# Kernel optimization log

Hardware: AMD Instinct MI355X
Metric: run time of the kernel (lower is better)

## Reference

```python
import jax, jax.numpy as jnp
import numpy as np

N_TYPES = 4
NEG_SLOPE = 0.01


def _conv(x, row, col, edge_type, edge_weight, W, b):
    # x: [N, d_in], W: [4, d_in, d_out], b: [d_out]
    N = x.shape[0]
    # in-degree based symmetric normalization (deg counted on col, as in source)
    deg = jax.ops.segment_sum(jnp.ones(col.shape[0], dtype=x.dtype), col, num_segments=N)
    deg_inv_sqrt = jnp.where(deg > 0, deg ** -0.5, jnp.zeros((), x.dtype))
    norm = deg_inv_sqrt[row] * deg_inv_sqrt[col] * edge_weight  # [E]
    # project all nodes by each of the 4 relation weights, then gather per edge
    # (equivalent to per-edge bmm x[col] @ W[edge_type], but avoids [E,d,d])
    xw = jnp.einsum('ni,tio->tno', x, W)          # [4, N, d_out]
    x_j = xw[edge_type, col] * norm[:, None]      # [E, d_out]
    out = jax.ops.segment_sum(x_j, row, num_segments=N) + b  # [N, d_out]
    # dropout omitted (eval mode / deterministic reference)
    return jax.nn.leaky_relu(out, negative_slope=NEG_SLOPE)


def setup_inputs() -> dict:
    key = jax.random.key(0)
    ks = jax.random.split(key, 10)
    N, d, E = 50000, 128, 625000
    x = jax.random.normal(ks[0], (N, d), dtype=jnp.float32)
    edge_index = jax.random.randint(ks[1], (2, E), 0, N, dtype=jnp.int64 if jax.config.jax_enable_x64 else jnp.int32)
    edge_type = jax.random.randint(ks[2], (E,), 0, N_TYPES)
    edge_attr = jax.random.uniform(ks[3], (E,), dtype=jnp.float32)
    # xavier_uniform for (4, d, d): gain=1, bound = sqrt(6/(d+d))
    bound = float(np.sqrt(6.0 / (d + d)))
    W1 = jax.random.uniform(ks[4], (N_TYPES, d, d), minval=-bound, maxval=bound, dtype=jnp.float32)
    W2 = jax.random.uniform(ks[5], (N_TYPES, d, d), minval=-bound, maxval=bound, dtype=jnp.float32)
    W3 = jax.random.uniform(ks[6], (N_TYPES, d, d), minval=-bound, maxval=bound, dtype=jnp.float32)
    b1 = jnp.zeros((d,), jnp.float32)
    b2 = jnp.zeros((d,), jnp.float32)
    b3 = jnp.zeros((d,), jnp.float32)
    return {"x": x, "edge_index": edge_index, "edge_type": edge_type, "edge_attr": edge_attr,
            "W1": W1, "b1": b1, "W2": W2, "b2": b2, "W3": W3, "b3": b3}


def reference(x, edge_index, edge_type, edge_attr, W1, b1, W2, b2, W3, b3):
    row, col = edge_index[0], edge_index[1]
    z1 = _conv(x, row, col, edge_type, edge_attr, W1, b1)
    z2 = _conv(z1, row, col, edge_type, edge_attr, W2, b2)
    z3 = _conv(z2, row, col, edge_type, edge_attr, W3, b3)
    return (x + z1 + z2 + z3) / 4
```

## Files before the change

### kernel.cpp

```cpp
#include <hip/hip_runtime.h>

#define DIM 128
#define SLOTS 64

typedef __attribute__((ext_vector_type(8))) short bf16x8;
typedef __attribute__((ext_vector_type(4))) float f32x4;
typedef __attribute__((ext_vector_type(2))) float f32x2;
typedef unsigned short u16;
typedef unsigned int u32;
typedef unsigned long long u64;

__device__ __forceinline__ float bf2f(u32 u) {
    return __builtin_bit_cast(float, u << 16);
}
__device__ __forceinline__ u16 f2bf(float f) {
    u32 u = __builtin_bit_cast(u32, f);
    u = (u + 0x7FFFu + ((u >> 16) & 1u)) >> 16;
    return (u16)u;
}
__device__ __forceinline__ u32 pack2bf(float a, float b) {
    return (u32)f2bf(a) | ((u32)f2bf(b) << 16);
}


__global__ __launch_bounds__(1024) void k_hist(const int* __restrict__ col, int E,
                                               int* __restrict__ part, int N) {
    __shared__ int hist[12544];
    int b = blockIdx.x;
    int range = b >> 3;
    int chunk = b & 7;
    int quarter = (N + 3) >> 2;
    int base = range * quarter;
    int hn = N - base; if (hn > quarter) hn = quarter;
    for (int i = threadIdx.x; i < hn; i += 1024) hist[i] = 0;
    __syncthreads();
    int e0 = (int)((long long)chunk * E / 8);
    int e1 = (int)((long long)(chunk + 1) * E / 8);
    for (int e = e0 + threadIdx.x; e < e1; e += 1024) {
        int c = col[e] - base;
        if ((u32)c < (u32)hn) atomicAdd(&hist[c], 1);
    }
    __syncthreads();
    int* dst = part + (size_t)b * quarter;
    for (int i = threadIdx.x; i < hn; i += 1024) dst[i] = hist[i];
}

__global__ void k_dis2(const int* __restrict__ part, float* __restrict__ dis, int N) {
    int i = blockIdx.x * 256 + threadIdx.x;
    if (i >= N) return;
    int quarter = (N + 3) >> 2;
    int range = i / quarter;
    int il = i - range * quarter;
    const int* p = part + ((size_t)range * 8) * quarter + il;
    int s = 0;
    #pragma unroll
    for (int b = 0; b < 8; b++) s += p[(size_t)b * quarter];
    dis[i] = s > 0 ? rsqrtf((float)s) : 0.f;
}


__global__ __launch_bounds__(256) void k_setup(const int* __restrict__ row, const int* __restrict__ col,
                                               const int* __restrict__ et, const float* __restrict__ ew,
                                               int E, int* __restrict__ fill,
                                               u64* __restrict__ ep,
                                               const float* __restrict__ x, u16* __restrict__ xb, int nx4,
                                               const float* __restrict__ W1, const float* __restrict__ W2,
                                               const float* __restrict__ W3,
                                               u16* __restrict__ Wt1, u16* __restrict__ Wt2,
                                               u16* __restrict__ Wt3, int nEb, int nXb) {
    int b = blockIdx.x, tid = threadIdx.x;
    if (b < nEb) {
        int e0 = (b * 256 + tid) * 4;
        #pragma unroll
        for (int i = 0; i < 4; i++) {
            int e = e0 + i;
            if (e < E) {
                int r = row[e], c = col[e];
                int pos = atomicAdd(&fill[r], 1);
                if (pos < SLOTS)
                    ep[(size_t)r * SLOTS + pos] =
                        ((u64)__builtin_bit_cast(u32, ew[e]) << 32) | (u32)((c << 8) | et[e]);
            }
        }
    } else if (b < nEb + nXb) {
        int i = (b - nEb) * 256 + tid;
        if (i < nx4) {
            float4 v = ((const float4*)x)[i];
            ushort4 o;
            o.x = f2bf(v.x); o.y = f2bf(v.y); o.z = f2bf(v.z); o.w = f2bf(v.w);
            ((ushort4*)xb)[i] = o;
        }
    } else {
        int b2 = b - nEb - nXb;
        const float* W = b2 < 256 ? W1 : (b2 < 512 ? W2 : W3);
        u16* Wt = b2 < 256 ? Wt1 : (b2 < 512 ? Wt2 : Wt3);
        int o = (b2 & 255) * 256 + tid;
        int chunk = o >> 10;
        int c = (o >> 3) & 127;
        int k = chunk * 8 + (o & 7);
        Wt[o] = f2bf(W[(k >> 7) * 16384 + (k & 127) * 128 + c]);
    }
}


__global__ __launch_bounds__(256) void k_norm(const int* __restrict__ fill,
                                              const float* __restrict__ dis,
                                              u64* __restrict__ ep, int N) {
    int wid = threadIdx.x >> 6, lane = threadIdx.x & 63;
    int n = blockIdx.x * 4 + wid;
    if (n >= N) return;
    int cnt = fill[n]; if (cnt > SLOTS) cnt = SLOTS;
    int padded = (cnt + 7) & ~7;
    float dn = dis[n];
    u64* eb = ep + (size_t)n * SLOTS;
    if (lane < cnt) {
        u64 q = eb[lane];
        u32 lo = (u32)q;
        float wgt = __builtin_bit_cast(float, (u32)(q >> 32)) * dn * dis[lo >> 8];
        eb[lane] = ((u64)__builtin_bit_cast(u32, wgt) << 32) | lo;
    } else if (lane < padded) {
        eb[lane] = 0;
    }
}


template <int MODE>
__global__ __launch_bounds__(1024, 2) void k_layer(const u16* __restrict__ src,
                                                   const int* __restrict__ fill,
                                                   const u64* __restrict__ ep,
                                                   const u16* __restrict__ Wt,
                                                   const float* __restrict__ bias,
                                                   const float* __restrict__ x0,
                                                   const u16* __restrict__ z1b,
                                                   const u16* __restrict__ z2b,
                                                   float* __restrict__ outf,
                                                   u16* __restrict__ outb, int N) {
    __shared__ u16 sA[16 * 512];
    int tid = threadIdx.x, wid = tid >> 6, lane = tid & 63;
    int n0 = blockIdx.x * 16;
    int n = n0 + wid;

    f32x2 a0 = {0.f, 0.f}, a1 = {0.f, 0.f}, a2 = {0.f, 0.f}, a3 = {0.f, 0.f};
    int cnt = 0;
    if (n < N) {
        cnt = fill[n];
        if (cnt > SLOTS) cnt = SLOTS;
    }
    u64 myq = ep[(size_t)n * SLOTS + lane];
    u32 mylo = (u32)myq;
    u32 mywu = (u32)(myq >> 32);
    const char* srcc = (const char*)src;

#define RL(x, i_) ((u32)__builtin_amdgcn_readlane((int)(x), (i_)))

#define EDGE(lo_, wu_, v_) { \
        float w_  = __builtin_bit_cast(float, (u32)(wu_)); \
        f32x2 vv_; \
        vv_[0] = __builtin_bit_cast(float, (v_) << 16); \
        vv_[1] = __builtin_bit_cast(float, (v_) & 0xFFFF0000u); \
        u32 t_ = (u32)(lo_) & 3u; \
        float w0_ = t_ == 0u ? w_ : 0.f; \
        float w1_ = t_ == 1u ? w_ : 0.f; \
        float w2_ = t_ == 2u ? w_ : 0.f; \
        float w3_ = t_ == 3u ? w_ : 0.f; \
        a0 = __builtin_elementwise_fma(vv_, (f32x2){w0_, w0_}, a0); \
        a1 = __builtin_elementwise_fma(vv_, (f32x2){w1_, w1_}, a1); \
        a2 = __builtin_elementwise_fma(vv_, (f32x2){w2_, w2_}, a2); \
        a3 = __builtin_elementwise_fma(vv_, (f32x2){w3_, w3_}, a3); }

    for (int j = 0; j < cnt; j += 8) {
        u32 lo[8], wu[8], v[8];
        #pragma unroll
        for (int i = 0; i < 8; i++) {
            lo[i] = RL(mylo, j + i);
            wu[i] = RL(mywu, j + i);
        }
        #pragma unroll
        for (int i = 0; i < 8; i++) {
            const u32* rowp = (const u32*)(srcc + (lo[i] & 0xFFFFFF00u));
            v[i] = rowp[lane];
        }
        #pragma unroll
        for (int i = 0; i < 8; i++)
            EDGE(lo[i], wu[i], v[i]);
    }
#undef EDGE
#undef RL

    {
        u32 X = (u32)((wid & 7) << 4);
        char* base = (char*)sA + wid * 1024;
        *(u32*)(base + ((lane * 4 + 0  ) ^ X)) = pack2bf(a0[0], a0[1]);
        *(u32*)(base + ((lane * 4 + 256) ^ X)) = pack2bf(a1[0], a1[1]);
        *(u32*)(base + ((lane * 4 + 512) ^ X)) = pack2bf(a2[0], a2[1]);
        *(u32*)(base + ((lane * 4 + 768) ^ X)) = pack2bf(a3[0], a3[1]);
    }
    __syncthreads();

    if (wid < 8) {
        int lr = lane & 15, lk = lane >> 4;
        u32 X = (u32)((lr & 7) << 4);
        const char* ab = (const char*)sA + lr * 1024;
        const u16* bb = Wt + lk * 1024 + (wid * 16 + lr) * 8;
        f32x4 acc = {};
        #pragma unroll
        for (int ks = 0; ks < 16; ks++) {
            bf16x8 af = *(const bf16x8*)(ab + ((ks * 64 + lk * 16) ^ X));
            bf16x8 bfv = *(const bf16x8*)(bb + ks * 4096);
            acc = __builtin_amdgcn_mfma_f32_16x16x32_bf16(af, bfv, acc, 0, 0, 0);
        }

        int colg = wid * 16 + lr;
        float bv = bias[colg];
        #pragma unroll
        for (int r = 0; r < 4; r++) {
            int nn = n0 + lk * 4 + r;
            if (nn < N) {
                size_t idx = (size_t)nn * DIM + colg;
                float v = acc[r] + bv;
                v = v > 0.f ? v : 0.01f * v;
                if (MODE == 1)
                    outf[idx] = 0.25f * (x0[idx] + bf2f(z1b[idx]) + bf2f(z2b[idx]) + v);
                else
                    outb[idx] = f2bf(v);
            }
        }
    }
}


extern "C" void kernel_launch(void* const* d_in, const int* in_sizes, int n_in,
                              void* d_out, int out_size, void* d_ws, size_t ws_size,
                              hipStream_t stream) {
    const float* x     = (const float*)d_in[0];
    const int*   eidx  = (const int*)d_in[1];
    const int*   etype = (const int*)d_in[2];
    const float* eattr = (const float*)d_in[3];
    const float* W1 = (const float*)d_in[4];
    const float* b1 = (const float*)d_in[5];
    const float* W2 = (const float*)d_in[6];
    const float* b2 = (const float*)d_in[7];
    const float* W3 = (const float*)d_in[8];
    const float* b3 = (const float*)d_in[9];

    const int E = in_sizes[2];
    const int N = in_sizes[0] / DIM;
    const int* row = eidx;
    const int* col = eidx + E;

    char* w = (char*)d_ws;
    size_t off = 0;
    auto alloc = [&](size_t bytes) { size_t o = off; off = (off + bytes + 255) & ~255ULL; return o; };
    int*   fill = (int*)(w + alloc((size_t)N * 4));
    float* dis  = (float*)(w + alloc((size_t)N * 4));
    int    quarter = (N + 3) >> 2;
    int*   part = (int*)(w + alloc((size_t)32 * quarter * 4));
    u64*   ep   = (u64*)(w + alloc((size_t)N * SLOTS * 8));
    u16*   xb   = (u16*)(w + alloc((size_t)N * DIM * 2));
    u16*   z1b  = (u16*)(w + alloc((size_t)N * DIM * 2));
    u16*   z2b  = (u16*)(w + alloc((size_t)N * DIM * 2));
    u16*   Wt1  = (u16*)(w + alloc(65536 * 2));
    u16*   Wt2  = (u16*)(w + alloc(65536 * 2));
    u16*   Wt3  = (u16*)(w + alloc(65536 * 2));

    hipMemsetAsync(fill, 0, (size_t)N * 4, stream);

    int nx4 = N * DIM / 4;
    int nEb = (E + 1023) / 1024;
    int nXb = (nx4 + 255) / 256;

    k_hist<<<32, 1024, 0, stream>>>(col, E, part, N);
    k_dis2<<<(N + 255) / 256, 256, 0, stream>>>(part, dis, N);
    k_setup<<<nEb + nXb + 768, 256, 0, stream>>>(row, col, etype, eattr, E, fill, ep,
                                                 x, xb, nx4, W1, W2, W3, Wt1, Wt2, Wt3, nEb, nXb);
    k_norm<<<(N + 3) / 4, 256, 0, stream>>>(fill, dis, ep, N);

    int grid = (N + 15) / 16;
    k_layer<0><<<grid, 1024, 0, stream>>>(xb,  fill, ep, Wt1, b1, nullptr, nullptr, nullptr, nullptr, z1b, N);
    k_layer<0><<<grid, 1024, 0, stream>>>(z1b, fill, ep, Wt2, b2, nullptr, nullptr, nullptr, nullptr, z2b, N);
    k_layer<1><<<grid, 1024, 0, stream>>>(z2b, fill, ep, Wt3, b3, x, z1b, z2b, (float*)d_out, nullptr, N);
}
```

Measured before the change: 234.5 us.

## Sort nodes by padded in-degree so each layer block gets balanced work

Adds a counting sort (bin, scan, place kernels) that orders nodes by their padded edge count in groups of 8. Each 16-node layer block then processes nodes with similar degree, which cuts wave imbalance inside a block before the shared-memory sync and MFMA. Output rows are scattered through the order table. This costs three extra small kernels and the loss of contiguous output rows, which weakens locality for the writes and the residual reads.

New measurement: 237.1 us. About the same (+1.1%).

```diff
diff --git a/kernel.cpp b/kernel.cpp
--- a/kernel.cpp
+++ b/kernel.cpp
@@ -123,10 +123,56 @@
     }
 }
 
+__global__ __launch_bounds__(256) void k_bin(const int* __restrict__ fill, int* __restrict__ nodeTmp,
+                                             int* __restrict__ partials, int N, int chunk) {
+    __shared__ int bins[9];
+    if (threadIdx.x < 9) bins[threadIdx.x] = 0;
+    __syncthreads();
+    int s = blockIdx.x * chunk;
+    int e = s + chunk; if (e > N) e = N;
+    for (int n = s + threadIdx.x; n < e; n += 256) {
+        int cnt = fill[n]; if (cnt > SLOTS) cnt = SLOTS;
+        int r = (cnt + 7) >> 3;
+        int lpos = atomicAdd(&bins[r], 1);
+        nodeTmp[n] = (r << 12) | lpos;
+    }
+    __syncthreads();
+    if (threadIdx.x < 9) partials[blockIdx.x * 9 + threadIdx.x] = bins[threadIdx.x];
+}
+
+__global__ __launch_bounds__(576) void k_scan9(const int* __restrict__ partials,
+                                               int* __restrict__ base) {
+    __shared__ int tot[9], start[9];
+    int wid = threadIdx.x >> 6;
+    int lane = threadIdx.x & 63;
+    int v = partials[lane * 9 + wid];
+    int incl = v;
+    for (int off = 1; off < 64; off <<= 1) {
+        int u = __shfl_up(incl, off);
+        if (lane >= off) incl += u;
+    }
+    if (lane == 63) tot[wid] = incl;
+    __syncthreads();
+    if (threadIdx.x == 0) { int s = 0; for (int r = 0; r < 9; r++) { start[r] = s; s += tot[r]; } }
+    __syncthreads();
+    base[lane * 9 + wid] = start[wid] + incl - v;
+}
+
+__global__ void k_place(const int* __restrict__ nodeTmp, const int* __restrict__ base,
+                        int* __restrict__ order, int N, int chunk) {
+    int n = blockIdx.x * 256 + threadIdx.x;
+    if (n < N) {
+        int v = nodeTmp[n];
+        int b = n / chunk;
+        int r = v >> 12, lpos = v & 4095;
+        order[base[b * 9 + r] + lpos] = (r << 20) | n;
+    }
+}
+
 
 template <int MODE>
 __global__ __launch_bounds__(1024, 2) void k_layer(const u16* __restrict__ src,
-                                                   const int* __restrict__ fill,
+                                                   const int* __restrict__ order,
                                                    const u64* __restrict__ ep,
                                                    const u16* __restrict__ Wt,
                                                    const float* __restrict__ bias,
@@ -136,17 +182,23 @@
                                                    float* __restrict__ outf,
                                                    u16* __restrict__ outb, int N) {
     __shared__ u16 sA[16 * 512];
+    __shared__ int sOrd[16];
     int tid = threadIdx.x, wid = tid >> 6, lane = tid & 63;
     int n0 = blockIdx.x * 16;
-    int n = n0 + wid;
+
+    if (wid == 0 && lane < 16) {
+        int gi = n0 + lane;
+        sOrd[lane] = gi < N ? (order[gi] & 0xFFFFF) : -1;
+    }
+
+    int gidx = n0 + wid;
+    int ov = gidx < N ? order[gidx] : 0;
+    int n = ov & 0xFFFFF;
+    int padded = gidx < N ? ((ov >> 20) << 3) : 0;
 
     f32x2 a0 = {0.f, 0.f}, a1 = {0.f, 0.f}, a2 = {0.f, 0.f}, a3 = {0.f, 0.f};
-    int cnt = 0;
-    if (n < N) {
-        cnt = fill[n];
-        if (cnt > SLOTS) cnt = SLOTS;
-    }
-    u64 myq = ep[(size_t)n * SLOTS + lane];
+    u64 myq = 0;
+    if (lane < padded) myq = ep[(size_t)n * SLOTS + lane];
     u32 mylo = (u32)myq;
     u32 mywu = (u32)(myq >> 32);
     const char* srcc = (const char*)src;
@@ -168,7 +220,7 @@
         a2 = __builtin_elementwise_fma(vv_, (f32x2){w2_, w2_}, a2); \
         a3 = __builtin_elementwise_fma(vv_, (f32x2){w3_, w3_}, a3); }
 
-    for (int j = 0; j < cnt; j += 8) {
+    for (int j = 0; j < padded; j += 8) {
         u32 lo[8], wu[8], v[8];
         #pragma unroll
         for (int i = 0; i < 8; i++) {
@@ -213,11 +265,11 @@
         int colg = wid * 16 + lr;
         float bv = bias[colg];
         #pragma unroll
-        for (int r = 0; r < 4; r++) {
-            int nn = n0 + lk * 4 + r;
-            if (nn < N) {
+        for (int q = 0; q < 4; q++) {
+            int nn = sOrd[lk * 4 + q];
+            if (nn >= 0) {
                 size_t idx = (size_t)nn * DIM + colg;
-                float v = acc[r] + bv;
+                float v = acc[q] + bv;
                 v = v > 0.f ? v : 0.01f * v;
                 if (MODE == 1)
                     outf[idx] = 0.25f * (x0[idx] + bf2f(z1b[idx]) + bf2f(z2b[idx]) + v);
@@ -251,32 +303,40 @@
     char* w = (char*)d_ws;
     size_t off = 0;
     auto alloc = [&](size_t bytes) { size_t o = off; off = (off + bytes + 255) & ~255ULL; return o; };
-    int*   fill = (int*)(w + alloc((size_t)N * 4));
-    float* dis  = (float*)(w + alloc((size_t)N * 4));
+    int*   fill    = (int*)(w + alloc((size_t)N * 4));
+    float* dis     = (float*)(w + alloc((size_t)N * 4));
     int    quarter = (N + 3) >> 2;
-    int*   part = (int*)(w + alloc((size_t)32 * quarter * 4));
-    u64*   ep   = (u64*)(w + alloc((size_t)N * SLOTS * 8));
-    u16*   xb   = (u16*)(w + alloc((size_t)N * DIM * 2));
-    u16*   z1b  = (u16*)(w + alloc((size_t)N * DIM * 2));
-    u16*   z2b  = (u16*)(w + alloc((size_t)N * DIM * 2));
-    u16*   Wt1  = (u16*)(w + alloc(65536 * 2));
-    u16*   Wt2  = (u16*)(w + alloc(65536 * 2));
-    u16*   Wt3  = (u16*)(w + alloc(65536 * 2));
+    int*   part    = (int*)(w + alloc((size_t)32 * quarter * 4));
+    int*   nodeTmp = (int*)(w + alloc((size_t)N * 4));
+    int*   partials= (int*)(w + alloc(64 * 9 * 4));
+    int*   basev   = (int*)(w + alloc(64 * 9 * 4));
+    int*   order   = (int*)(w + alloc((size_t)N * 4));
+    u64*   ep      = (u64*)(w + alloc((size_t)N * SLOTS * 8));
+    u16*   xb      = (u16*)(w + alloc((size_t)N * DIM * 2));
+    u16*   z1b     = (u16*)(w + alloc((size_t)N * DIM * 2));
+    u16*   z2b     = (u16*)(w + alloc((size_t)N * DIM * 2));
+    u16*   Wt1     = (u16*)(w + alloc(65536 * 2));
+    u16*   Wt2     = (u16*)(w + alloc(65536 * 2));
+    u16*   Wt3     = (u16*)(w + alloc(65536 * 2));
 
     hipMemsetAsync(fill, 0, (size_t)N * 4, stream);
 
     int nx4 = N * DIM / 4;
     int nEb = (E + 1023) / 1024;
     int nXb = (nx4 + 255) / 256;
+    int chunk = (N + 63) / 64;
 
     k_hist<<<32, 1024, 0, stream>>>(col, E, part, N);
     k_dis2<<<(N + 255) / 256, 256, 0, stream>>>(part, dis, N);
     k_setup<<<nEb + nXb + 768, 256, 0, stream>>>(row, col, etype, eattr, E, fill, ep,
                                                  x, xb, nx4, W1, W2, W3, Wt1, Wt2, Wt3, nEb, nXb);
     k_norm<<<(N + 3) / 4, 256, 0, stream>>>(fill, dis, ep, N);
+    k_bin<<<64, 256, 0, stream>>>(fill, nodeTmp, partials, N, chunk);
+    k_scan9<<<1, 576, 0, stream>>>(partials, basev);
+    k_place<<<(N + 255) / 256, 256, 0, stream>>>(nodeTmp, basev, order, N, chunk);
 
     int grid = (N + 15) / 16;
-    k_layer<0><<<grid, 1024, 0, stream>>>(xb,  fill, ep, Wt1, b1, nullptr, nullptr, nullptr, nullptr, z1b, N);
-    k_layer<0><<<grid, 1024, 0, stream>>>(z1b, fill, ep, Wt2, b2, nullptr, nullptr, nullptr, nullptr, z2b, N);
-    k_layer<1><<<grid, 1024, 0, stream>>>(z2b, fill, ep, Wt3, b3, x, z1b, z2b, (float*)d_out, nullptr, N);
-}
+    k_layer<0><<<grid, 1024, 0, stream>>>(xb,  order, ep, Wt1, b1, nullptr, nullptr, nullptr, nullptr, z1b, N);
+    k_layer<0><<<grid, 1024, 0, stream>>>(z1b, order, ep, Wt2, b2, nullptr, nullptr, nullptr, nullptr, z2b, N);
+    k_layer<1><<<grid, 1024, 0, stream>>>(z2b, order, ep, Wt3, b3, x, z1b, z2b, (float*)d_out, nullptr, N);
+}
```
